# Kernel tuning notes

Measured on AMD Instinct MI355X. Metric: run time of the kernel, lower is better.

Reference implementation:

```python
import jax, jax.numpy as jnp
import numpy as np

N_SEQ, L_RES, Q_STATES = 8192, 256, 21


def setup_inputs() -> dict:
    key = jax.random.key(0)
    k_x, k_h, k_j, k_perm = jax.random.split(key, 4)
    # One-hot encoded MSA: [N, L, q]
    aa_idx = jax.random.randint(k_x, (N_SEQ, L_RES), 0, Q_STATES)
    X = jax.nn.one_hot(aa_idx, Q_STATES, dtype=jnp.float32)
    # Model parameters (torch.randn init in the original module)
    h = jax.random.normal(k_h, (L_RES, Q_STATES), dtype=jnp.float32)
    J = jax.random.normal(k_j, (L_RES, Q_STATES, L_RES, Q_STATES), dtype=jnp.float32)
    # Order of residues to update during the Gibbs sweep (a permutation of 0..L-1)
    residue_idxs = jax.random.permutation(k_perm, L_RES)
    return {"X": X, "residue_idxs": residue_idxs, "h": h, "J": J, "beta": 1.0}


def reference(X, residue_idxs, h, J, beta):
    """One sequential Gibbs sweep over the residues (plmDCA.forward).

    For each residue i (in the given order):
      logits_i = h[i] + X_flat @ J[i].reshape(q, L*q).T   (equiv. einsum below)
      X[:, i]  = one_hot(sample ~ softmax(beta * logits_i))
    The loop is a true data-dependent recurrence -> lax.scan.
    """
    n, l, q = X.shape
    n_steps = residue_idxs.shape[0]
    keys = jax.random.split(jax.random.key(42), n_steps)

    def step(X_cur, inp):
        i, k = inp
        J_i = jnp.take(J, i, axis=0)  # [q, L, q]
        h_i = jnp.take(h, i, axis=0)  # [q]
        # [N, q] cavity logits for residue i
        logits = h_i + jnp.einsum('nlb,alb->na', X_cur, J_i)
        # multinomial over softmax(beta * logits) == categorical(beta * logits)
        s = jax.random.categorical(k, beta * logits, axis=-1)  # [N]
        X_cur = X_cur.at[:, i, :].set(jax.nn.one_hot(s, q, dtype=X_cur.dtype))
        return X_cur, None

    X_out, _ = jax.lax.scan(step, X, (residue_idxs, keys))
    return X_out
```

## Files before the change

### kernel.cpp

```cpp
#include <hip/hip_runtime.h>
#include <stdint.h>
#include <math.h>


#define NSEQ 8192
#define LRES 256
#define QST  21
#define KC   288
#define SPB  32
#define NTHREADS (SPB * QST)

__device__ __forceinline__ uint32_t rotl32(uint32_t v, uint32_t r) {
  return (v << r) | (v >> (32u - r));
}

__device__ __forceinline__ void threefry2x32(uint32_t k0, uint32_t k1,
                                             uint32_t c0, uint32_t c1,
                                             uint32_t& o0, uint32_t& o1) {
  uint32_t ks2 = k0 ^ k1 ^ 0x1BD11BDAu;
  uint32_t x0 = c0 + k0;
  uint32_t x1 = c1 + k1;
#define TF_ROUND(r) { x0 += x1; x1 = rotl32(x1, r); x1 ^= x0; }
  TF_ROUND(13u) TF_ROUND(15u) TF_ROUND(26u) TF_ROUND(6u)
  x0 += k1;  x1 += ks2 + 1u;
  TF_ROUND(17u) TF_ROUND(29u) TF_ROUND(16u) TF_ROUND(24u)
  x0 += ks2; x1 += k0 + 2u;
  TF_ROUND(13u) TF_ROUND(15u) TF_ROUND(26u) TF_ROUND(6u)
  x0 += k0;  x1 += k1 + 3u;
  TF_ROUND(17u) TF_ROUND(29u) TF_ROUND(16u) TF_ROUND(24u)
  x0 += k1;  x1 += ks2 + 4u;
  TF_ROUND(13u) TF_ROUND(15u) TF_ROUND(26u) TF_ROUND(6u)
  x0 += ks2; x1 += k0 + 5u;
#undef TF_ROUND
  o0 = x0; o1 = x1;
}

__device__ __forceinline__ float gumbel_f32(uint32_t bits) {
  float f = __uint_as_float((bits >> 9) | 0x3f800000u) - 1.0f;
  float u = fmaxf(1.17549435e-38f, f + 1.17549435e-38f);
  float w = (float)log((double)u);
  float t = -w;
  float g = -(float)log((double)t);
  return g;
}

__global__ __launch_bounds__(NTHREADS)
void gibbs_sweep(const float* __restrict__ X, const int* __restrict__ order,
                 const float* __restrict__ h, const float* __restrict__ J,
                 const float* __restrict__ betaPtr, float* __restrict__ out) {
  __shared__ int   bst[LRES][SPB];
  __shared__ float vals[QST][SPB];

  const int nl  = threadIdx.x;
  const int a   = threadIdx.y;
  const int tid = nl + SPB * a;
  const int n0  = blockIdx.x * SPB;
  const int n   = n0 + nl;
  const float beta = betaPtr[0];

  for (int idx = tid; idx < SPB * LRES; idx += NTHREADS) {
    int s = idx >> 8;
    int l = idx & 255;
    const float* xp = X + ((size_t)(n0 + s) * LRES + l) * QST;
    int b = 0;
#pragma unroll
    for (int j = 0; j < QST; ++j) b = (xp[j] > 0.5f) ? j : b;
    bst[l][s] = b;
  }
  __syncthreads();

  for (int t = 0; t < LRES; ++t) {
    const int i = order[t];
    const float* Jrow = J + ((size_t)i * QST + a) * (size_t)(LRES * QST);

    float tot = 0.0f, part = 0.0f;
    int bnd = KC;
#pragma unroll 8
    for (int l = 0; l < LRES; ++l) {
      int b = bst[l][nl];
      int k = l * QST + b;
      float jv = Jrow[l * QST + b];
      bool  cr = (k >= bnd);
      float tp = tot + part;
      tot  = cr ? tp   : tot;
      part = cr ? 0.0f : part;
      bnd  = cr ? bnd + KC : bnd;
      part += jv;
    }
    tot += part;

    float lo = h[i * QST + a] + tot;

    uint32_t kk0, kk1, o0, o1;
    threefry2x32(0u, 42u, 0u, (uint32_t)t, kk0, kk1);
    threefry2x32(kk0, kk1, 0u, (uint32_t)(n * QST + a), o0, o1);
    float g = gumbel_f32(o0 ^ o1);

    vals[a][nl] = g + beta * lo;
    __syncthreads();

    if (a == 0) {
      float best = vals[0][nl];
      int bi = 0;
#pragma unroll
      for (int j = 1; j < QST; ++j) {
        float vv = vals[j][nl];
        if (vv > best) { best = vv; bi = j; }
      }
      bst[i][nl] = bi;
    }
    __syncthreads();
  }

  const size_t base = (size_t)n0 * LRES * QST;
  for (int idx = tid; idx < SPB * LRES * QST; idx += NTHREADS) {
    int s   = idx / (LRES * QST);
    int rem = idx - s * (LRES * QST);
    int l   = rem / QST;
    int j   = rem - l * QST;
    out[base + idx] = (bst[l][s] == j) ? 1.0f : 0.0f;
  }
}

extern "C" void kernel_launch(void* const* d_in, const int* in_sizes, int n_in,
                              void* d_out, int out_size, void* d_ws, size_t ws_size,
                              hipStream_t stream) {
  const float* X     = (const float*)d_in[0];
  const int*   order = (const int*)  d_in[1];
  const float* h     = (const float*)d_in[2];
  const float* J     = (const float*)d_in[3];
  const float* beta  = (const float*)d_in[4];
  float* out = (float*)d_out;

  dim3 grid(NSEQ / SPB);
  dim3 block(SPB, QST);
  hipLaunchKernelGGL(gibbs_sweep, grid, block, 0, stream, X, order, h, J, beta, out);
}
```

Baseline: 6.037 ms.

## Pack sequence state into bytes, shrink blocks, fully unroll with compile-time chunk boundaries

Sequences per block drop from 32 to 8, giving 1024 blocks of 168 threads instead of 256 blocks of 672, so more blocks can spread across CUs. The per-sequence state is packed four residues per 32-bit word in shared memory, and the inner loop over L is fully unrolled. The summation-chunk boundaries for the blocked reduction come from a constexpr table, so most iterations become a plain add instead of a compare-and-select. The full unroll and constant table raise code size and possibly register pressure, and smaller blocks give less reuse of the broadcast per-step setup.

Result: slower. 9.727 ms (+61.1%).

```diff
diff --git a/kernel.cpp b/kernel.cpp
--- a/kernel.cpp
+++ b/kernel.cpp
@@ -6,9 +6,20 @@
 #define NSEQ 8192
 #define LRES 256
 #define QST  21
-#define KC   288
-#define SPB  32
+#define SPB  8
 #define NTHREADS (SPB * QST)
+
+struct KcTbl {
+  unsigned char thr[LRES];
+  constexpr KcTbl() : thr() {
+    for (int i = 0; i < LRES; ++i) thr[i] = 255;
+    for (int m = 1; m < 19; ++m) {
+      int l = (288 * m) / 21;
+      thr[l] = (unsigned char)(288 * m - 21 * l);
+    }
+  }
+};
+static constexpr KcTbl KC_TBL{};
 
 __device__ __forceinline__ uint32_t rotl32(uint32_t v, uint32_t r) {
   return (v << r) | (v >> (32u - r));
@@ -48,8 +59,8 @@
 void gibbs_sweep(const float* __restrict__ X, const int* __restrict__ order,
                  const float* __restrict__ h, const float* __restrict__ J,
                  const float* __restrict__ betaPtr, float* __restrict__ out) {
-  __shared__ int   bst[LRES][SPB];
-  __shared__ float vals[QST][SPB];
+  __shared__ uint32_t sbst[(LRES / 4) * SPB];
+  __shared__ float    vals[QST][SPB];
 
   const int nl  = threadIdx.x;
   const int a   = threadIdx.y;
@@ -58,34 +69,46 @@
   const int n   = n0 + nl;
   const float beta = betaPtr[0];
 
-  for (int idx = tid; idx < SPB * LRES; idx += NTHREADS) {
-    int s = idx >> 8;
-    int l = idx & 255;
-    const float* xp = X + ((size_t)(n0 + s) * LRES + l) * QST;
-    int b = 0;
+  for (int idx = tid; idx < (LRES / 4) * SPB; idx += NTHREADS) {
+    int s  = idx & (SPB - 1);
+    int wg = idx >> 3;
+    uint32_t w = 0;
 #pragma unroll
-    for (int j = 0; j < QST; ++j) b = (xp[j] > 0.5f) ? j : b;
-    bst[l][s] = b;
+    for (int j = 0; j < 4; ++j) {
+      int l = 4 * wg + j;
+      const float* xp = X + ((size_t)(n0 + s) * LRES + l) * QST;
+      int b = 0;
+#pragma unroll
+      for (int q = 0; q < QST; ++q) b = (xp[q] > 0.5f) ? q : b;
+      w |= ((uint32_t)b) << (8 * j);
+    }
+    sbst[wg * SPB + s] = w;
   }
   __syncthreads();
 
   for (int t = 0; t < LRES; ++t) {
     const int i = order[t];
-    const float* Jrow = J + ((size_t)i * QST + a) * (size_t)(LRES * QST);
+    const uint32_t rowoff = (uint32_t)(i * QST + a) * (uint32_t)(LRES * QST);
 
     float tot = 0.0f, part = 0.0f;
-    int bnd = KC;
-#pragma unroll 8
-    for (int l = 0; l < LRES; ++l) {
-      int b = bst[l][nl];
-      int k = l * QST + b;
-      float jv = Jrow[l * QST + b];
-      bool  cr = (k >= bnd);
-      float tp = tot + part;
-      tot  = cr ? tp   : tot;
-      part = cr ? 0.0f : part;
-      bnd  = cr ? bnd + KC : bnd;
-      part += jv;
+#pragma unroll
+    for (int lg = 0; lg < LRES / 4; ++lg) {
+      uint32_t w = sbst[lg * SPB + nl];
+#pragma unroll
+      for (int j = 0; j < 4; ++j) {
+        const int l = 4 * lg + j;
+        uint32_t b = (w >> (8 * j)) & 0xffu;
+        float jv = J[rowoff + (uint32_t)(l * QST) + b];
+        const int thr = KC_TBL.thr[l];
+        if (thr == 255) {
+          part += jv;
+        } else if (thr == 0) {
+          tot += part; part = jv;
+        } else {
+          if ((int)b >= thr) { tot += part; part = jv; }
+          else               { part += jv; tot += part; part = 0.0f; }
+        }
+      }
     }
     tot += part;
 
@@ -103,11 +126,12 @@
       float best = vals[0][nl];
       int bi = 0;
 #pragma unroll
-      for (int j = 1; j < QST; ++j) {
-        float vv = vals[j][nl];
-        if (vv > best) { best = vv; bi = j; }
+      for (int q = 1; q < QST; ++q) {
+        float vv = vals[q][nl];
+        if (vv > best) { best = vv; bi = q; }
       }
-      bst[i][nl] = bi;
+      unsigned char* bp = reinterpret_cast<unsigned char*>(sbst);
+      bp[((i >> 2) * SPB + nl) * 4 + (i & 3)] = (unsigned char)bi;
     }
     __syncthreads();
   }
@@ -117,8 +141,10 @@
     int s   = idx / (LRES * QST);
     int rem = idx - s * (LRES * QST);
     int l   = rem / QST;
-    int j   = rem - l * QST;
-    out[base + idx] = (bst[l][s] == j) ? 1.0f : 0.0f;
+    int q   = rem - l * QST;
+    uint32_t w = sbst[(l >> 2) * SPB + s];
+    int b = (int)((w >> (8 * (l & 3))) & 0xffu);
+    out[base + idx] = (b == q) ? 1.0f : 0.0f;
   }
 }
 
```
